# Optimization experiments

Hardware: AMD Instinct MI355X
Metric: run time of the kernel (lower is better)

The kernel has to match this reference:

```python
import jax, jax.numpy as jnp
import numpy as np
import math

LATENT = 64
COMP = 20
EM_ITERS = 5
GAMMA1 = 1.0  # 1/sqrt(gamma), gamma=1
LOG_NORM_C = -0.5 * math.log(2.0 * math.pi)


def setup_inputs() -> dict:
    key = jax.random.key(0)
    k1, k2, k3 = jax.random.split(key, 3)
    z = jax.random.normal(k1, (64, 8192, LATENT), dtype=jnp.float32)
    # small causal adjacency so (I - A) and the inverses are well conditioned
    A = jax.random.normal(k2, (LATENT, LATENT), dtype=jnp.float32) * 0.05
    init_idx = jax.random.randint(k3, (64, COMP), 0, 8192)
    return {"z": z, "A": A, "init_idx": init_idx}


def _em_step(X, pi, mean, trace, IA):
    # X: [B,N,L], pi/trace: [B,K], mean: [B,K,L], IA = I - A: [L,L]
    B, N, L = X.shape
    # gaussian_log_prob(X, mean) with logvar=0, summed over L, expanded as
    # -0.5*||x-m||^2 + L*c, computed without materializing a [B,N,K,L] tensor
    sq_x = jnp.sum(X * X, axis=-1)                      # [B,N]
    sq_m = jnp.sum(mean * mean, axis=-1)                # [B,K]
    cross = jnp.einsum('bnl,bkl->bnk', X, mean)         # [B,N,K]
    term_x = -0.5 * (sq_x[:, :, None] - 2.0 * cross + sq_m[:, None, :]) + L * LOG_NORM_C
    # gaussian_log_prob(causal(mean), 0, logvar=log(trace) broadcast over L)
    cm = jnp.einsum('bkl,lm->bkm', mean, IA)            # causal(mean)
    lt = jnp.log(trace)                                  # [B,K]
    term_c = -0.5 * (L * lt + jnp.sum(cm * cm, axis=-1) / trace) + L * LOG_NORM_C
    ll = term_x + jnp.log(pi)[:, None, :] + term_c[:, None, :]   # [B,N,K]
    post = jax.nn.softmax(ll, axis=-1)
    Nk = jnp.sum(post, axis=1)                           # [B,K]
    Nk = jnp.where(Nk == 0.0, jnp.asarray(1e-22, Nk.dtype), Nk)
    new_trace = GAMMA1 * jnp.ones_like(Nk)
    # std_causal = causal(I*trace) = trace*(I-A); trace is gamma1 for every
    # (b,k), so the [B,K,L,L] inverse collapses to one shared [L,L] inverse.
    I = jnp.eye(L, dtype=X.dtype)
    M = jnp.linalg.inv(I + (GAMMA1 ** 2) * (IA @ IA.T))
    new_pi = Nk / jnp.sum(Nk, axis=-1, keepdims=True)    # fix_pi=False
    new_mean = jnp.einsum('bnk,bnl->bkl', post, X) / Nk[:, :, None]
    new_mean = jnp.einsum('bkl,lm->bkm', new_mean, M)
    return new_pi, new_mean, new_trace


def reference(z, A, init_idx):
    # EM-based Gaussian-mixture prior (get_unsupervised_prior) of GMVAE
    B, N, L = z.shape
    I = jnp.eye(L, dtype=z.dtype)
    IA = I - A  # linear CausalEncoder: causal(x) = x @ (I - A)
    pi = jnp.full((B, COMP), 1.0 / COMP, dtype=z.dtype)
    trace = jnp.ones((B, COMP), dtype=z.dtype)
    # initial inverse: inv(I + (1/trace) * sig_cas @ sig_cas.T), trace == 1
    M0 = jnp.linalg.inv(I + IA @ IA.T)
    mean = jnp.take_along_axis(z, init_idx[:, :, None], axis=1)  # [B,K,L]
    mean = jnp.einsum('bkl,lm->bkm', mean, M0)
    for _ in range(EM_ITERS):
        pi, mean, trace = _em_step(z, pi, mean, trace, IA)
    return pi, mean, trace
```

## Files before the change

kernel.cpp:

```cpp
#include <hip/hip_runtime.h>
#include <math.h>

#define BB 64
#define NN 8192
#define LL 64
#define KK 20
#define TILE 128
#define NT 8
#define CHUNKS 8
#define ZSB 72
#define ZTS 136
#define PTTS 136
#define NSS 68

typedef float f32x4 __attribute__((ext_vector_type(4)));
typedef short s16x8 __attribute__((ext_vector_type(8)));

#define MFMA_BF16 __builtin_amdgcn_mfma_f32_16x16x32_bf16

__device__ __forceinline__ unsigned short f2bf(float f) {
    unsigned int u = __float_as_uint(f);
    u += 0x7fffu + ((u >> 16) & 1u);
    return (unsigned short)(u >> 16);
}
__device__ __forceinline__ float bf2f(unsigned short h) {
    return __uint_as_float(((unsigned int)h) << 16);
}


__global__ __launch_bounds__(256) void k_setup(const float* __restrict__ A,
                                               float* __restrict__ IA,
                                               float* __restrict__ M) {
    __shared__ __align__(16) float sS[64][NSS];
    __shared__ __align__(16) float sXa[64][NSS];
    __shared__ __align__(16) float sXb[64][NSS];
    __shared__ __align__(16) float sT[64][NSS];
    __shared__ float rowsum[64];
    __shared__ float alpha_s;
    int t = threadIdx.x;
    int r0 = (t >> 4) << 2;
    int c0 = (t & 15) << 2;

    for (int i = t; i < 4096; i += 256) {
        int r = i >> 6, c = i & 63;
        float v = (r == c ? 1.0f : 0.0f) - A[i];
        IA[i] = v;
        sT[c][r] = v;
    }
    __syncthreads();
    {
        float s[4][4];
        #pragma unroll
        for (int a = 0; a < 4; ++a)
            #pragma unroll
            for (int b = 0; b < 4; ++b) s[a][b] = 0.f;
        #pragma unroll 4
        for (int l = 0; l < 64; ++l) {
            float4 u = *(const float4*)&sT[l][r0];
            float4 v = *(const float4*)&sT[l][c0];
            float uu[4] = {u.x, u.y, u.z, u.w};
            float vv[4] = {v.x, v.y, v.z, v.w};
            #pragma unroll
            for (int a = 0; a < 4; ++a)
                #pragma unroll
                for (int b = 0; b < 4; ++b) s[a][b] += uu[a] * vv[b];
        }
        #pragma unroll
        for (int a = 0; a < 4; ++a) {
            int r = r0 + a;
            float4 w;
            w.x = s[a][0] + (r == c0 + 0 ? 1.f : 0.f);
            w.y = s[a][1] + (r == c0 + 1 ? 1.f : 0.f);
            w.z = s[a][2] + (r == c0 + 2 ? 1.f : 0.f);
            w.w = s[a][3] + (r == c0 + 3 ? 1.f : 0.f);
            *(float4*)&sS[r][c0] = w;
        }
    }
    __syncthreads();
    if (t < 64) {
        float sm = 0.f;
        #pragma unroll 4
        for (int c = 0; c < 64; c += 4) {
            float4 v = *(const float4*)&sS[t][c];
            sm += fabsf(v.x) + fabsf(v.y) + fabsf(v.z) + fabsf(v.w);
        }
        rowsum[t] = sm;
    }
    __syncthreads();
    if (t == 0) {
        float mx = rowsum[0];
        for (int i = 1; i < 64; ++i) mx = fmaxf(mx, rowsum[i]);
        alpha_s = 2.0f / (1.0f + mx);
    }
    __syncthreads();
    float alpha = alpha_s;
    for (int i = t; i < 4096; i += 256) {
        int r = i >> 6, c = i & 63;
        sXa[r][c] = (r == c) ? alpha : 0.f;
    }
    __syncthreads();

    float* X  = &sXa[0][0];
    float* Xn = &sXb[0][0];
    for (int it = 0; it < 8; ++it) {
        {
            float s[4][4];
            #pragma unroll
            for (int a = 0; a < 4; ++a)
                #pragma unroll
                for (int b = 0; b < 4; ++b) s[a][b] = 0.f;
            #pragma unroll 4
            for (int k = 0; k < 64; ++k) {
                float4 u = *(const float4*)&sS[k][r0];
                float4 v = *(const float4*)&X[k * NSS + c0];
                float uu[4] = {u.x, u.y, u.z, u.w};
                float vv[4] = {v.x, v.y, v.z, v.w};
                #pragma unroll
                for (int a = 0; a < 4; ++a)
                    #pragma unroll
                    for (int b = 0; b < 4; ++b) s[a][b] += uu[a] * vv[b];
            }
            #pragma unroll
            for (int a = 0; a < 4; ++a)
                *(float4*)&sT[r0 + a][c0] = (float4){s[a][0], s[a][1], s[a][2], s[a][3]};
        }
        __syncthreads();
        {
            float s[4][4];
            #pragma unroll
            for (int a = 0; a < 4; ++a)
                #pragma unroll
                for (int b = 0; b < 4; ++b) s[a][b] = 0.f;
            #pragma unroll 4
            for (int k = 0; k < 64; ++k) {
                float4 u = *(const float4*)&X[k * NSS + r0];
                float4 v = *(const float4*)&sT[k][c0];
                float uu[4] = {u.x, u.y, u.z, u.w};
                float vv[4] = {v.x, v.y, v.z, v.w};
                #pragma unroll
                for (int a = 0; a < 4; ++a)
                    #pragma unroll
                    for (int b = 0; b < 4; ++b) s[a][b] += uu[a] * vv[b];
            }
            #pragma unroll
            for (int a = 0; a < 4; ++a) {
                float4 xo = *(const float4*)&X[(r0 + a) * NSS + c0];
                float4 w;
                w.x = 2.f * xo.x - s[a][0];
                w.y = 2.f * xo.y - s[a][1];
                w.z = 2.f * xo.z - s[a][2];
                w.w = 2.f * xo.w - s[a][3];
                *(float4*)&Xn[(r0 + a) * NSS + c0] = w;
            }
        }
        __syncthreads();
        float* tmp = X; X = Xn; Xn = tmp;
    }
    for (int i = t; i < 4096; i += 256)
        M[i] = X[(i >> 6) * NSS + (i & 63)];
}

__global__ __launch_bounds__(64) void k_init(const float* __restrict__ z,
                                             const int* __restrict__ idxs,
                                             const float* __restrict__ M,
                                             const float* __restrict__ IA,
                                             float* __restrict__ out_mean,
                                             float* __restrict__ bias,
                                             float* __restrict__ nk,
                                             float* __restrict__ macc,
                                             int* __restrict__ cnt) {
    int k = blockIdx.x, b = blockIdx.y;
    int l = threadIdx.x;
    int bk = b * KK + k;
    __shared__ float srow[64];
    __shared__ float smean[64];
    int idx = idxs[bk];
    srow[l] = z[((size_t)b * NN + idx) * LL + l];
    __syncthreads();
    float nm = 0.f;
    #pragma unroll 8
    for (int m = 0; m < 64; ++m) nm += srow[m] * M[m * 64 + l];
    out_mean[(size_t)bk * LL + l] = nm;
    smean[l] = nm;
    __syncthreads();
    float cm = 0.f;
    #pragma unroll 8
    for (int m = 0; m < 64; ++m) cm += smean[m] * IA[m * 64 + l];
    float sqm = nm * nm;
    float sqc = cm * cm;
    for (int off = 32; off > 0; off >>= 1) {
        sqm += __shfl_down(sqm, off);
        sqc += __shfl_down(sqc, off);
    }
    if (l == 0) {
        bias[bk] = logf(1.0f / KK) - 0.5f * (sqm + sqc);
        nk[bk] = 0.f;
        if (k == 0) cnt[b] = 0;
    }
    macc[(size_t)bk * LL + l] = 0.f;
}

__global__ __launch_bounds__(512, 4) void k_empass(const float* __restrict__ z,
                                                   float* __restrict__ mean,
                                                   float* __restrict__ bias,
                                                   float* __restrict__ nk,
                                                   float* __restrict__ macc,
                                                   int* __restrict__ cnt,
                                                   const float* __restrict__ M,
                                                   const float* __restrict__ IA,
                                                   float* __restrict__ out_pi,
                                                   float* __restrict__ out_trace) {
    __shared__ __align__(16) unsigned short mhl[2][32][ZSB];
    __shared__ __align__(16) unsigned short zT[64][ZTS];
    __shared__ __align__(16) unsigned short ptT[32][PTTS];
    __shared__ __align__(16) float bias_s[32];
    __shared__ float nkred[8][KK];
    __shared__ int isLast;
    int t = threadIdx.x;
    int lane = t & 63;
    int q = t >> 6;
    int ln = lane & 15;
    int lg4 = lane >> 4;
    int b = blockIdx.y;
    size_t zbase = ((size_t)b * NN + (size_t)blockIdx.x * (TILE * NT)) * LL;
    int zr = q * 16 + ln;
    int fbase = zr * 16 + 2 * lg4;

    for (int i = t; i < KK * LL; i += 512) {
        float f = mean[(size_t)b * KK * LL + i];
        int k = i >> 6, c = i & 63;
        unsigned short h = f2bf(f);
        mhl[0][k][c] = h;
        mhl[1][k][c] = f2bf(f - bf2f(h));
    }
    for (int i = 20 * ZSB + t; i < 32 * ZSB; i += 512) {
        (&mhl[0][0][0])[i] = 0;
        (&mhl[1][0][0])[i] = 0;
    }
    if (t < 32) bias_s[t] = (t < KK) ? bias[b * KK + t] : -1e30f;

    const float4* zg = (const float4*)(z + zbase);
    float4 pf[4];
    pf[0] = zg[fbase];
    pf[1] = zg[fbase + 1];
    pf[2] = zg[fbase + 8];
    pf[3] = zg[fbase + 9];
    __syncthreads();
    float4 b0 = *(const float4*)&bias_s[lg4 * 4];
    float4 b1 = *(const float4*)&bias_s[16 + lg4 * 4];
    s16x8 mf[8];
    #pragma unroll
    for (int ks = 0; ks < 2; ++ks) {
        int kc = ks * 32 + lg4 * 8;
        mf[ks * 4 + 0] = *(const s16x8*)&mhl[0][ln][kc];
        mf[ks * 4 + 1] = *(const s16x8*)&mhl[1][ln][kc];
        mf[ks * 4 + 2] = *(const s16x8*)&mhl[0][16 + ln][kc];
        mf[ks * 4 + 3] = *(const s16x8*)&mhl[1][16 + ln][kc];
    }

    int ct = q & 3;
    int chb = 2 * (q >> 2);
    f32x4 bacc0 = {0.f, 0.f, 0.f, 0.f};
    f32x4 bacc1 = {0.f, 0.f, 0.f, 0.f};
    float nkp0[4] = {0.f, 0.f, 0.f, 0.f};
    float nkp1[4] = {0.f, 0.f, 0.f, 0.f};

    for (int tt = 0; tt < NT; ++tt) {
        s16x8 zh0, zl0, zh1, zl1;
        #pragma unroll
        for (int i = 0; i < 2; ++i) {
            float4 v = pf[i];
            float vv[4] = {v.x, v.y, v.z, v.w};
            #pragma unroll
            for (int j = 0; j < 4; ++j) {
                unsigned short h = f2bf(vv[j]);
                zh0[4 * i + j] = (short)h;
                zl0[4 * i + j] = (short)f2bf(vv[j] - bf2f(h));
            }
        }
        #pragma unroll
        for (int i = 0; i < 2; ++i) {
            float4 v = pf[2 + i];
            float vv[4] = {v.x, v.y, v.z, v.w};
            #pragma unroll
            for (int j = 0; j < 4; ++j) {
                unsigned short h = f2bf(vv[j]);
                zh1[4 * i + j] = (short)h;
                zl1[4 * i + j] = (short)f2bf(vv[j] - bf2f(h));
            }
        }
        if (tt + 1 < NT) {
            size_t o = (size_t)(tt + 1) * 2048;
            pf[0] = zg[o + fbase];
            pf[1] = zg[o + fbase + 1];
            pf[2] = zg[o + fbase + 8];
            pf[3] = zg[o + fbase + 9];
        }
        #pragma unroll
        for (int e = 0; e < 8; ++e) {
            zT[8 * lg4 + e][zr]      = (unsigned short)zh0[e];
            zT[32 + 8 * lg4 + e][zr] = (unsigned short)zh1[e];
        }

        f32x4 acc0 = (f32x4){b0.x, b0.y, b0.z, b0.w};
        f32x4 acc1 = (f32x4){b1.x, b1.y, b1.z, b1.w};
        acc0 = MFMA_BF16(mf[0], zh0, acc0, 0, 0, 0);
        acc0 = MFMA_BF16(mf[1], zh0, acc0, 0, 0, 0);
        acc0 = MFMA_BF16(mf[0], zl0, acc0, 0, 0, 0);
        acc0 = MFMA_BF16(mf[4], zh1, acc0, 0, 0, 0);
        acc0 = MFMA_BF16(mf[5], zh1, acc0, 0, 0, 0);
        acc0 = MFMA_BF16(mf[4], zl1, acc0, 0, 0, 0);
        acc1 = MFMA_BF16(mf[2], zh0, acc1, 0, 0, 0);
        acc1 = MFMA_BF16(mf[3], zh0, acc1, 0, 0, 0);
        acc1 = MFMA_BF16(mf[2], zl0, acc1, 0, 0, 0);
        acc1 = MFMA_BF16(mf[6], zh1, acc1, 0, 0, 0);
        acc1 = MFMA_BF16(mf[7], zh1, acc1, 0, 0, 0);
        acc1 = MFMA_BF16(mf[6], zl1, acc1, 0, 0, 0);

        {
            float m = fmaxf(fmaxf(fmaxf(acc0[0], acc0[1]), fmaxf(acc0[2], acc0[3])),
                            fmaxf(fmaxf(acc1[0], acc1[1]), fmaxf(acc1[2], acc1[3])));
            m = fmaxf(m, __shfl_xor(m, 16));
            m = fmaxf(m, __shfl_xor(m, 32));
            float e0[4], e1[4];
            float sm = 0.f;
            #pragma unroll
            for (int j = 0; j < 4; ++j) {
                e0[j] = __expf(acc0[j] - m); sm += e0[j];
                e1[j] = __expf(acc1[j] - m); sm += e1[j];
            }
            sm += __shfl_xor(sm, 16);
            sm += __shfl_xor(sm, 32);
            float inv = 1.0f / sm;
            #pragma unroll
            for (int j = 0; j < 4; ++j) {
                float p0 = e0[j] * inv;
                float p1 = e1[j] * inv;
                nkp0[j] += p0;
                nkp1[j] += p1;
                ptT[lg4 * 4 + j][zr] = f2bf(p0);
                ptT[16 + lg4 * 4 + j][zr] = f2bf(p1);
            }
        }
        __syncthreads();

        #pragma unroll
        for (int chi = 0; chi < 2; ++chi) {
            int rr = (chb + chi) * 32 + lg4 * 8;
            s16x8 zb  = *(const s16x8*)&zT[ct * 16 + ln][rr];
            s16x8 af0 = *(const s16x8*)&ptT[ln][rr];
            s16x8 af1 = *(const s16x8*)&ptT[16 + ln][rr];
            bacc0 = MFMA_BF16(af0, zb, bacc0, 0, 0, 0);
            bacc1 = MFMA_BF16(af1, zb, bacc1, 0, 0, 0);
        }
        __syncthreads();
    }

    #pragma unroll
    for (int j = 0; j < 4; ++j) {
        nkp0[j] += __shfl_xor(nkp0[j], 1);
        nkp0[j] += __shfl_xor(nkp0[j], 2);
        nkp0[j] += __shfl_xor(nkp0[j], 4);
        nkp0[j] += __shfl_xor(nkp0[j], 8);
        nkp1[j] += __shfl_xor(nkp1[j], 1);
        nkp1[j] += __shfl_xor(nkp1[j], 2);
        nkp1[j] += __shfl_xor(nkp1[j], 4);
        nkp1[j] += __shfl_xor(nkp1[j], 8);
    }
    if (ln == 0) {
        #pragma unroll
        for (int j = 0; j < 4; ++j) nkred[q][lg4 * 4 + j] = nkp0[j];
        if (lg4 == 0) {
            #pragma unroll
            for (int j = 0; j < 4; ++j) nkred[q][16 + j] = nkp1[j];
        }
    }

    int col = ct * 16 + ln;
    #pragma unroll
    for (int reg = 0; reg < 4; ++reg) {
        int comp = lg4 * 4 + reg;
        atomicAdd(&macc[((size_t)b * KK + comp) * LL + col], bacc0[reg]);
    }
    if (lg4 == 0) {
        #pragma unroll
        for (int reg = 0; reg < 4; ++reg)
            atomicAdd(&macc[((size_t)b * KK + 16 + reg) * LL + col], bacc1[reg]);
    }
    __syncthreads();
    if (t < KK) {
        float sum = 0.f;
        #pragma unroll
        for (int w = 0; w < 8; ++w) sum += nkred[w][t];
        atomicAdd(&nk[b * KK + t], sum);
    }
    __syncthreads();
    if (t == 0) {
        __threadfence();
        int old = atomicAdd(&cnt[b], 1);
        isLast = (old == CHUNKS - 1) ? 1 : 0;
    }
    __syncthreads();
    if (!isLast) return;

    if (q < 4) {
        float* fs = (float*)&zT[0][0];
        float* sraw = fs + q * 160;
        float* smean = sraw + 64;
        int l = lane;
        #pragma unroll
        for (int kc5 = 0; kc5 < 5; ++kc5) {
            int comp = kc5 * 4 + q;
            int bk = b * KK + comp;
            size_t mb = (size_t)bk * LL;
            float nkv = 0.f;
            if (l == 0) nkv = atomicExch(&nk[bk], 0.f);
            nkv = __shfl(nkv, 0);
            float nkc = fmaxf(nkv, 1e-22f);
            float raw = atomicExch(&macc[mb + l], 0.f) / nkc;
            sraw[l] = raw;
            float nm = 0.f;
            #pragma unroll 8
            for (int m = 0; m < 64; ++m) nm += sraw[m] * M[m * 64 + l];
            mean[mb + l] = nm;
            smean[l] = nm;
            float cm = 0.f;
            #pragma unroll 8
            for (int m = 0; m < 64; ++m) cm += smean[m] * IA[m * 64 + l];
            float sqm = nm * nm;
            float sqc = cm * cm;
            #pragma unroll
            for (int off = 32; off > 0; off >>= 1) {
                sqm += __shfl_down(sqm, off);
                sqc += __shfl_down(sqc, off);
            }
            if (l == 0) {
                float pi = nkc * (1.0f / NN);
                bias[bk] = logf(pi) - 0.5f * (sqm + sqc);
                out_pi[bk] = pi;
                out_trace[bk] = 1.0f;
            }
        }
    }
    if (t == 0) cnt[b] = 0;
}

extern "C" void kernel_launch(void* const* d_in, const int* in_sizes, int n_in,
                              void* d_out, int out_size, void* d_ws, size_t ws_size,
                              hipStream_t stream) {
    const float* z = (const float*)d_in[0];
    const float* A = (const float*)d_in[1];
    const int* idxs = (const int*)d_in[2];

    float* out_pi = (float*)d_out;
    float* out_mean = out_pi + BB * KK;
    float* out_trace = out_mean + (size_t)BB * KK * LL;

    float* ws = (float*)d_ws;
    float* IA = ws;
    float* M = ws + 4096;
    float* bias = ws + 8192;
    float* nk = ws + 9472;
    float* macc = ws + 10752;
    int* cnt = (int*)(ws + 92672);

    k_setup<<<1, 256, 0, stream>>>(A, IA, M);
    k_init<<<dim3(KK, BB), 64, 0, stream>>>(z, idxs, M, IA, out_mean, bias, nk, macc, cnt);
    for (int it = 0; it < 5; ++it) {
        k_empass<<<dim3(CHUNKS, BB), 512, 0, stream>>>(z, out_mean, bias, nk, macc,
                                                       cnt, M, IA, out_pi, out_trace);
    }
}
```

Measured before the change: 306.7 us.

## Stage z tiles into LDS via async global_load_lds instead of register prefetch

Replaces the per-thread register prefetch of the next z tile with direct global-to-LDS loads into a swizzled fp32 staging buffer, issued after a barrier and overlapped with the MFMA work. Threads then read their rows from LDS. This frees prefetch registers and uses hardware async copies. In exchange it adds 32 KB of LDS per block, which may cut occupancy under launch_bounds(512,4), plus an extra barrier and a full vmcnt wait at the end of each iteration.

```diff
diff --git a/kernel.cpp b/kernel.cpp
--- a/kernel.cpp
+++ b/kernel.cpp
@@ -210,6 +210,7 @@
                                                    const float* __restrict__ IA,
                                                    float* __restrict__ out_pi,
                                                    float* __restrict__ out_trace) {
+    __shared__ __align__(16) float zf32[TILE][64];
     __shared__ __align__(16) unsigned short mhl[2][32][ZSB];
     __shared__ __align__(16) unsigned short zT[64][ZTS];
     __shared__ __align__(16) unsigned short ptT[32][PTTS];
@@ -224,7 +225,25 @@
     int b = blockIdx.y;
     size_t zbase = ((size_t)b * NN + (size_t)blockIdx.x * (TILE * NT)) * LL;
     int zr = q * 16 + ln;
-    int fbase = zr * 16 + 2 * lg4;
+
+#define STAGE_TILE(tt)                                                         \
+    {                                                                          \
+        const char* gtb = (const char*)(z + zbase + (size_t)(tt) * (TILE*LL)); \
+        char* lb = (char*)&zf32[0][0];                                         \
+        _Pragma("unroll")                                                      \
+        for (int j = 0; j < 4; ++j) {                                          \
+            int chunk = q * 4 + j;                                             \
+            int row_ = chunk * 4 + (lane >> 4);                                \
+            int sg_ = (lane & 15) ^ (row_ & 7);                                \
+            __builtin_amdgcn_global_load_lds(                                  \
+                (const __attribute__((address_space(1))) unsigned int*)(gtb + row_ * 256 + sg_ * 16), \
+                (__attribute__((address_space(3))) unsigned int*)(lb + chunk * 1024), \
+                16, 0, 0);                                                     \
+        }                                                                      \
+    }
+#define ZF_PTR(row_, s_) ((const float4*)((const char*)&zf32[0][0] + (row_) * 256 + (((s_) ^ ((row_) & 7)) * 16)))
+
+    STAGE_TILE(0);
 
     for (int i = t; i < KK * LL; i += 512) {
         float f = mean[(size_t)b * KK * LL + i];
@@ -238,14 +257,10 @@
         (&mhl[1][0][0])[i] = 0;
     }
     if (t < 32) bias_s[t] = (t < KK) ? bias[b * KK + t] : -1e30f;
-
-    const float4* zg = (const float4*)(z + zbase);
-    float4 pf[4];
-    pf[0] = zg[fbase];
-    pf[1] = zg[fbase + 1];
-    pf[2] = zg[fbase + 8];
-    pf[3] = zg[fbase + 9];
-    __syncthreads();
+    asm volatile("s_waitcnt vmcnt(0) lgkmcnt(0)" ::: "memory");
+    __builtin_amdgcn_sched_barrier(0);
+    __syncthreads();
+
     float4 b0 = *(const float4*)&bias_s[lg4 * 4];
     float4 b1 = *(const float4*)&bias_s[16 + lg4 * 4];
     s16x8 mf[8];
@@ -266,36 +281,30 @@
     float nkp1[4] = {0.f, 0.f, 0.f, 0.f};
 
     for (int tt = 0; tt < NT; ++tt) {
+        float4 f0 = *ZF_PTR(zr, 2 * lg4);
+        float4 f1 = *ZF_PTR(zr, 2 * lg4 + 1);
+        float4 f2 = *ZF_PTR(zr, 8 + 2 * lg4);
+        float4 f3 = *ZF_PTR(zr, 9 + 2 * lg4);
         s16x8 zh0, zl0, zh1, zl1;
-        #pragma unroll
-        for (int i = 0; i < 2; ++i) {
-            float4 v = pf[i];
-            float vv[4] = {v.x, v.y, v.z, v.w};
-            #pragma unroll
-            for (int j = 0; j < 4; ++j) {
-                unsigned short h = f2bf(vv[j]);
-                zh0[4 * i + j] = (short)h;
-                zl0[4 * i + j] = (short)f2bf(vv[j] - bf2f(h));
-            }
-        }
-        #pragma unroll
-        for (int i = 0; i < 2; ++i) {
-            float4 v = pf[2 + i];
-            float vv[4] = {v.x, v.y, v.z, v.w};
-            #pragma unroll
-            for (int j = 0; j < 4; ++j) {
-                unsigned short h = f2bf(vv[j]);
-                zh1[4 * i + j] = (short)h;
-                zl1[4 * i + j] = (short)f2bf(vv[j] - bf2f(h));
-            }
-        }
-        if (tt + 1 < NT) {
-            size_t o = (size_t)(tt + 1) * 2048;
-            pf[0] = zg[o + fbase];
-            pf[1] = zg[o + fbase + 1];
-            pf[2] = zg[o + fbase + 8];
-            pf[3] = zg[o + fbase + 9];
-        }
+        {
+            float v0[8] = {f0.x, f0.y, f0.z, f0.w, f1.x, f1.y, f1.z, f1.w};
+            float v1[8] = {f2.x, f2.y, f2.z, f2.w, f3.x, f3.y, f3.z, f3.w};
+            #pragma unroll
+            for (int j = 0; j < 8; ++j) {
+                unsigned short h = f2bf(v0[j]);
+                zh0[j] = (short)h;
+                zl0[j] = (short)f2bf(v0[j] - bf2f(h));
+                unsigned short g = f2bf(v1[j]);
+                zh1[j] = (short)g;
+                zl1[j] = (short)f2bf(v1[j] - bf2f(g));
+            }
+        }
+        asm volatile("s_waitcnt lgkmcnt(0)" ::: "memory");
+        __builtin_amdgcn_sched_barrier(0);
+        __syncthreads();
+
+        if (tt + 1 < NT) STAGE_TILE(tt + 1);
+
         #pragma unroll
         for (int e = 0; e < 8; ++e) {
             zT[8 * lg4 + e][zr]      = (unsigned short)zh0[e];
@@ -353,6 +362,8 @@
             bacc0 = MFMA_BF16(af0, zb, bacc0, 0, 0, 0);
             bacc1 = MFMA_BF16(af1, zb, bacc1, 0, 0, 0);
         }
+        asm volatile("s_waitcnt vmcnt(0) lgkmcnt(0)" ::: "memory");
+        __builtin_amdgcn_sched_barrier(0);
         __syncthreads();
     }
 
@@ -443,6 +454,8 @@
         }
     }
     if (t == 0) cnt[b] = 0;
+#undef STAGE_TILE
+#undef ZF_PTR
 }
 
 extern "C" void kernel_launch(void* const* d_in, const int* in_sizes, int n_in,
```

New measurement: 342.5 us. 1.12x slower.
